# Optimization experiments

Hardware: AMD Instinct MI355X
Metric: run time of the kernel (lower is better)

## Reference

```python
import jax, jax.numpy as jnp
import numpy as np


def setup_inputs() -> dict:
    key = jax.random.key(0)
    k1, k2 = jax.random.split(key)
    x = jax.random.normal(k1, (64, 32, 32, 128), dtype=jnp.float32)
    embeddings = jax.random.normal(k2, (128, 1024), dtype=jnp.float32)  # (embedding_dim, num_embeddings)
    return {"x": x, "embeddings": embeddings}


def reference(x, embeddings):
    d = embeddings.shape[0]
    flat = x.reshape(-1, d)  # [N, d]
    # squared L2 distances: ||f||^2 + ||e||^2 - 2 f.e
    similarity = flat @ embeddings  # [N, K]
    distances = (jnp.sum(flat * flat, axis=1, keepdims=True)
                 + jnp.sum(embeddings * embeddings, axis=0)
                 - 2.0 * similarity)
    idx = jnp.argmin(distances, axis=1)  # [N]
    # gather codes (equivalent to one_hot @ embeddings^T)
    quantized = embeddings.T[idx].reshape(x.shape)
    # straight-through estimator
    quantized = x + jax.lax.stop_gradient(quantized - x)
    return quantized
```

## Files before the change

kernel.cpp:

```cpp
#include <hip/hip_runtime.h>


#define NROWS 65536
#define DDIM 128
#define KCODES 1024
#define MARGIN1 0.30f
#define MARGIN2 1e-3f

typedef __attribute__((ext_vector_type(8))) short short8;
typedef __attribute__((ext_vector_type(16))) float f32x16;

__device__ inline ushort f2bf(float f) {
    union { float f; unsigned u; } v; v.f = f;
    unsigned r = v.u + 0x7fffu + ((v.u >> 16) & 1u);
    return (ushort)(r >> 16);
}
__device__ inline float bf2f(ushort b) {
    union { unsigned u; float f; } v; v.u = ((unsigned)b) << 16;
    return v.f;
}

__device__ inline void gload_lds16(const uint4* g, uint4* lds) {
    __builtin_amdgcn_global_load_lds((const __attribute__((address_space(1))) void*)g,
                                     (__attribute__((address_space(3))) void*)lds,
                                     16, 0, 0);
}

__global__ void k_prep(const float* __restrict__ x, const float* __restrict__ e,
                       float* __restrict__ et, float* __restrict__ nrm,
                       double* __restrict__ nrm64, uint4* __restrict__ epq,
                       unsigned* __restrict__ nhl, uint4* __restrict__ xp) {
    const int gid = blockIdx.x * blockDim.x + threadIdx.x;

    {
        int lane = gid & 63, c = (gid >> 6) & 7, rt = gid >> 9;
        int row = rt * 32 + (lane & 31);
        int kbase = c * 16 + ((lane >> 5) << 3);
        const float4* xr4 = reinterpret_cast<const float4*>(x + (size_t)row * DDIM + kbase);
        float4 u = xr4[0], v = xr4[1];
        float fv[8] = {u.x, u.y, u.z, u.w, v.x, v.y, v.z, v.w};
        union { ushort s[8]; uint4 q; } pk;
        #pragma unroll
        for (int j = 0; j < 8; ++j) pk.s[j] = f2bf(fv[j]);
        xp[gid] = pk.q;
    }

    if (gid < 131072) {
        int d = gid >> 10, k = gid & 1023;
        et[k * DDIM + d] = e[gid];
    }

    if (gid < 16384) {
        int lane = gid & 63, c = (gid >> 6) & 7, nt = gid >> 9;
        int col = nt * 32 + (lane & 31);
        int kbase = c * 16 + ((lane >> 5) << 3);
        union { ushort s[8]; uint4 q; } pk;
        #pragma unroll
        for (int j = 0; j < 8; ++j)
            pk.s[j] = f2bf(e[(kbase + j) * KCODES + col]);
        epq[(size_t)nt * 512 + c * 64 + lane] = pk.q;
    }

    if (gid >= 32768 && gid < 32768 + 8192) {
        int t2 = gid - 32768;
        int k = t2 >> 3, part = t2 & 7;
        double s = 0.0;
        #pragma unroll
        for (int j = 0; j < 16; ++j) {
            double v = (double)e[(part * 16 + j) * KCODES + k];
            s = fma(v, v, s);
        }
        #pragma unroll
        for (int m = 1; m < 8; m <<= 1) s += __shfl_xor(s, m);
        if (part == 0) {
            nrm64[k] = s; nrm[k] = (float)s;
            float t0 = (float)(-0.5 * s);
            ushort hb = f2bf(t0);
            ushort lb = f2bf(t0 - bf2f(hb));
            nhl[k] = (unsigned)hb | ((unsigned)lb << 16);
        }
    }
}

__global__ __launch_bounds__(256, 3) void k_argmin32(const uint4* __restrict__ xp,
                                                     const uint4* __restrict__ epq,
                                                     const unsigned* __restrict__ nhl,
                                                     unsigned* __restrict__ pb1,
                                                     float* __restrict__ pb2) {
    __shared__ uint4 sbuf[2048];
    __shared__ unsigned snhl[128];

    const int tid = threadIdx.x;
    const int lane = tid & 63;
    const int w = tid >> 6;
    const int kq = blockIdx.x & 7;
    const int rt = (blockIdx.x >> 3) * 4 + w;
    const int lrow = lane & 31;
    const int lgrp = lane >> 5;

    #pragma unroll
    for (int i = 0; i < 8; ++i)
        gload_lds16(epq + (size_t)kq * 2048 + i * 256 + tid,
                    &sbuf[i * 256 + (w << 6)]);
    if (tid < 32)
        gload_lds16(reinterpret_cast<const uint4*>(nhl) + kq * 32 + tid,
                    reinterpret_cast<uint4*>(snhl) + tid);

    short8 ah[8];
    #pragma unroll
    for (int c = 0; c < 8; ++c) {
        union { uint4 q; short8 s; } u;
        u.q = xp[(size_t)rt * 512 + c * 64 + lane];
        ah[c] = u.s;
    }
    short8 bx = {0, 0, 0, 0, 0, 0, 0, 0};
    if (lgrp == 0) { bx[0] = (short)0x3F80; bx[1] = (short)0x3F80; }

    int cidlow[16];
    #pragma unroll
    for (int r = 0; r < 16; ++r)
        cidlow[r] = (((r & 3) + ((r >> 2) << 3)) | (lgrp << 2));

    asm volatile("s_waitcnt vmcnt(0)" ::: "memory");
    __syncthreads();

    float kb1 = -3.4e38f, kb2 = -3.4e38f;

    for (int t = 0; t < 4; ++t) {
        f32x16 acc;
        #pragma unroll
        for (int r = 0; r < 16; ++r) acc[r] = 0.f;

        #pragma unroll
        for (int c = 0; c < 8; ++c) {
            union { uint4 q; short8 s; } ef;
            ef.q = sbuf[t * 512 + c * 64 + lane];
            acc = __builtin_amdgcn_mfma_f32_32x32x16_bf16(ef.s, ah[c], acc, 0, 0, 0);
        }
        unsigned hl = snhl[t * 32 + lrow];
        short8 ax = {0, 0, 0, 0, 0, 0, 0, 0};
        if (lgrp == 0) { ax[0] = (short)(hl & 0xFFFF); ax[1] = (short)(hl >> 16); }
        acc = __builtin_amdgcn_mfma_f32_32x32x16_bf16(ax, bx, acc, 0, 0, 0);

        #pragma unroll
        for (int r = 0; r < 16; ++r) {
            unsigned cid = (unsigned)((t << 5) | cidlow[r]);
            float key = __uint_as_float((__float_as_uint(acc[r]) & 0xFFFFFF00u) | cid);
            kb2 = fmaxf(kb2, fminf(key, kb1));
            kb1 = fmaxf(kb1, key);
        }
    }

    float o1 = __shfl_xor(kb1, 32);
    float o2 = __shfl_xor(kb2, 32);
    float m1k = fmaxf(kb1, o1);
    float m2k = fmaxf(fmaxf(kb2, o2), fminf(kb1, o1));

    if (lane < 32) {
        size_t o = (size_t)kq * NROWS + rt * 32 + lrow;
        pb1[o] = __float_as_uint(m1k);
        pb2[o] = m2k;
    }
}

__global__ void k_merge(const unsigned* __restrict__ pb1, const float* __restrict__ pb2,
                        int* __restrict__ idx, int* __restrict__ wlc,
                        int* __restrict__ wl) {
    int r = blockIdx.x * blockDim.x + threadIdx.x;
    float best = -3.4e38f, sec = -3.4e38f; int bq = 0;
    #pragma unroll
    for (int q = 0; q < 8; ++q) {
        float k1 = __uint_as_float(pb1[(size_t)q * NROWS + r]);
        float k2 = pb2[(size_t)q * NROWS + r];
        bool t = k1 > best;
        sec = fmaxf(sec, fmaxf(k2, t ? best : k1));
        bq = t ? q : bq;
        best = t ? k1 : best;
    }
    unsigned ub = __float_as_uint(best);
    int code = bq * 128 + (int)(ub & 255u);
    float m1 = __uint_as_float(ub & 0xFFFFFF00u);
    float m2 = __uint_as_float(__float_as_uint(sec) & 0xFFFFFF00u);
    idx[r] = code;
    if (2.f * (m1 - m2) < MARGIN1) {
        int slot = atomicAdd(wlc, 1);
        wl[slot] = r;
    }
}

__global__ __launch_bounds__(256) void k_rescan(const float* __restrict__ x,
                                                const float* __restrict__ e,
                                                const float* __restrict__ nrm,
                                                const int* __restrict__ wlc,
                                                const int* __restrict__ wl,
                                                int* __restrict__ idx,
                                                int* __restrict__ wl2c,
                                                int* __restrict__ wl2) {
    __shared__ float xs[4][DDIM];
    __shared__ float rb1[4][256], rb2[4][256];
    __shared__ int   ri[4][256];
    const int tid = threadIdx.x, lane = tid & 63, wv = tid >> 6;
    const int n = *wlc;

    for (int i0 = blockIdx.x * 4; i0 < n; i0 += gridDim.x * 4) {
        if (tid < 128) {
            int j = tid >> 5, d4 = tid & 31;
            int ii = i0 + j;
            int row = wl[ii < n ? ii : i0];
            *reinterpret_cast<float4*>(&xs[j][d4 * 4]) =
                *reinterpret_cast<const float4*>(&x[(size_t)row * DDIM + d4 * 4]);
        }
        __syncthreads();

        float acc[4][4];
        #pragma unroll
        for (int kk = 0; kk < 4; ++kk)
            #pragma unroll
            for (int j = 0; j < 4; ++j) acc[kk][j] = 0.f;

        for (int d = 0; d < DDIM; d += 2) {
            float xv0[4], xv1[4];
            #pragma unroll
            for (int j = 0; j < 4; ++j) { xv0[j] = xs[j][d]; xv1[j] = xs[j][d + 1]; }
            #pragma unroll
            for (int kk = 0; kk < 4; ++kk) {
                float ev0 = e[d * KCODES + kk * 256 + tid];
                float ev1 = e[(d + 1) * KCODES + kk * 256 + tid];
                #pragma unroll
                for (int j = 0; j < 4; ++j) {
                    acc[kk][j] = fmaf(ev0, xv0[j], acc[kk][j]);
                    acc[kk][j] = fmaf(ev1, xv1[j], acc[kk][j]);
                }
            }
        }

        #pragma unroll
        for (int j = 0; j < 4; ++j) {
            float b1 = 3.4e38f, b2 = 3.4e38f; int bi = 0;
            #pragma unroll
            for (int kk = 0; kk < 4; ++kk) {
                int k = kk * 256 + tid;
                float s = fmaf(-2.f, acc[kk][j], nrm[k]);
                if (s < b1) { b2 = b1; b1 = s; bi = k; }
                else b2 = fminf(b2, s);
            }
            rb1[j][tid] = b1; rb2[j][tid] = b2; ri[j][tid] = bi;
        }
        __syncthreads();

        {
            float b1 = 3.4e38f, b2 = 3.4e38f; int bi = 0;
            #pragma unroll
            for (int p = 0; p < 4; ++p) {
                int t2 = lane + p * 64;
                float o1 = rb1[wv][t2], o2 = rb2[wv][t2]; int oi = ri[wv][t2];
                bool take = (o1 < b1) || (o1 == b1 && oi < bi);
                float loser = take ? b1 : o1;
                b1 = take ? o1 : b1;
                bi = take ? oi : bi;
                b2 = fminf(fminf(b2, o2), loser);
            }
            #pragma unroll
            for (int m = 1; m < 64; m <<= 1) {
                float o1 = __shfl_xor(b1, m);
                float o2 = __shfl_xor(b2, m);
                int   oi = __shfl_xor(bi, m);
                bool take = (o1 < b1) || (o1 == b1 && oi < bi);
                float loser = take ? b1 : o1;
                b1 = take ? o1 : b1;
                bi = take ? oi : bi;
                b2 = fminf(fminf(b2, o2), loser);
            }
            if (lane == 0 && i0 + wv < n) {
                int row = wl[i0 + wv];
                idx[row] = bi;
                if (b2 - b1 < MARGIN2) {
                    int slot = atomicAdd(wl2c, 1);
                    wl2[slot] = row;
                }
            }
        }
        __syncthreads();
    }
}

__global__ __launch_bounds__(256) void k_fix(const float* __restrict__ x,
                                             const float* __restrict__ e,
                                             const double* __restrict__ nrm64,
                                             const int* __restrict__ wlc,
                                             const int* __restrict__ wl,
                                             int* __restrict__ idx) {
    __shared__ float  xs[DDIM];
    __shared__ double w1[4]; __shared__ int wi[4];
    const int tid = threadIdx.x;
    const int lane = tid & 63;
    const int wv = tid >> 6;
    const int n = *wlc;

    for (int i = blockIdx.x; i < n; i += gridDim.x) {
        const int row = wl[i];
        if (tid < DDIM) xs[tid] = x[(size_t)row * DDIM + tid];
        __syncthreads();

        double dot[4] = {0.0, 0.0, 0.0, 0.0};
        for (int d0 = 0; d0 < DDIM; d0 += 8) {
            float ef[8][4];
            #pragma unroll
            for (int dd = 0; dd < 8; ++dd)
                #pragma unroll
                for (int kk = 0; kk < 4; ++kk)
                    ef[dd][kk] = e[(d0 + dd) * KCODES + tid + kk * 256];
            #pragma unroll
            for (int dd = 0; dd < 8; ++dd) {
                double xv = (double)xs[d0 + dd];
                #pragma unroll
                for (int kk = 0; kk < 4; ++kk)
                    dot[kk] = fma(xv, (double)ef[dd][kk], dot[kk]);
            }
        }

        double bb1 = 1e300; int bbi = 0;
        #pragma unroll
        for (int kk = 0; kk < 4; ++kk) {
            int k = tid + kk * 256;
            double sc = nrm64[k] - 2.0 * dot[kk];
            if (sc < bb1) { bb1 = sc; bbi = k; }
        }
        #pragma unroll
        for (int m = 1; m < 64; m <<= 1) {
            double o1 = __shfl_xor(bb1, m);
            int    oi = __shfl_xor(bbi, m);
            bool take = (o1 < bb1) || (o1 == bb1 && oi < bbi);
            bb1 = take ? o1 : bb1;
            bbi = take ? oi : bbi;
        }
        if (lane == 0) { w1[wv] = bb1; wi[wv] = bbi; }
        __syncthreads();
        if (tid == 0) {
            double f1 = w1[0]; int fi = wi[0];
            #pragma unroll
            for (int j = 1; j < 4; ++j) {
                bool take = (w1[j] < f1) || (w1[j] == f1 && wi[j] < fi);
                f1 = take ? w1[j] : f1;
                fi = take ? wi[j] : fi;
            }
            idx[row] = fi;
        }
        __syncthreads();
    }
}

__global__ void k_gather(const float* __restrict__ x, const float* __restrict__ et,
                         const int* __restrict__ idxp, float* __restrict__ out) {
    int gid = blockIdx.x * blockDim.x + threadIdx.x;
    int row = gid >> 5, d4 = gid & 31;
    float4 q = reinterpret_cast<const float4*>(et)[(size_t)idxp[row] * 32 + d4];
    float4 xv = reinterpret_cast<const float4*>(x)[gid];
    float4 o;
    o.x = xv.x + (q.x - xv.x);
    o.y = xv.y + (q.y - xv.y);
    o.z = xv.z + (q.z - xv.z);
    o.w = xv.w + (q.w - xv.w);
    reinterpret_cast<float4*>(out)[gid] = o;
}

extern "C" void kernel_launch(void* const* d_in, const int* in_sizes, int n_in,
                              void* d_out, int out_size, void* d_ws, size_t ws_size,
                              hipStream_t stream) {
    const float* x = (const float*)d_in[0];
    const float* e = (const float*)d_in[1];
    float* out = (float*)d_out;

    double*   nrm64 = (double*)d_ws;
    float*    et    = (float*)d_ws + 2048;
    float*    nrm   = et + 131072;
    int*      idx   = (int*)(nrm + 1024);
    int*      wlc   = idx + NROWS;
    int*      wl    = wlc + 4;
    int*      wl2   = wl + NROWS;
    uint4*    epq   = (uint4*)(wl2 + NROWS);
    unsigned* nhl   = (unsigned*)(epq + 16384);
    unsigned* pb1   = nhl + 1024;
    float*    pb2   = (float*)(pb1 + 8 * NROWS);
    uint4*    xp    = (uint4*)d_out;

    hipMemsetAsync(wlc, 0, 2 * sizeof(int), stream);

    k_prep<<<4096, 256, 0, stream>>>(x, e, et, nrm, nrm64, epq, nhl, xp);
    k_argmin32<<<4096, 256, 0, stream>>>(xp, epq, nhl, pb1, pb2);
    k_merge<<<NROWS / 256, 256, 0, stream>>>(pb1, pb2, idx, wlc, wl);
    k_rescan<<<768, 256, 0, stream>>>(x, e, nrm, wlc, wl, idx, wlc + 1, wl2);
    k_fix<<<64, 256, 0, stream>>>(x, e, nrm64, wlc + 1, wl2, idx);
    k_gather<<<(NROWS * 32) / 256, 256, 0, stream>>>(x, et, idx, out);
}
```

Baseline: 101.7 us.

## Process two row tiles per wave in argmin and merge rescan with fp64 fix

The MFMA argmin kernel now computes two 32-row tiles per wave. Each codebook fragment read from LDS is reused across both tiles, and the grid is halved. The single-precision rescan and the separate fp64 fix kernel are merged into one fp64 rescan, which removes a launch and the second worklist. The counter memset is folded into the prep kernel. In exchange, every rescanned row now does double-precision work, and the argmin kernel needs more registers per wave.

New measurement: 95.35 us. -6.2%, faster.

```diff
diff --git a/kernel.cpp b/kernel.cpp
--- a/kernel.cpp
+++ b/kernel.cpp
@@ -5,7 +5,6 @@
 #define DDIM 128
 #define KCODES 1024
 #define MARGIN1 0.30f
-#define MARGIN2 1e-3f
 
 typedef __attribute__((ext_vector_type(8))) short short8;
 typedef __attribute__((ext_vector_type(16))) float f32x16;
@@ -29,8 +28,11 @@
 __global__ void k_prep(const float* __restrict__ x, const float* __restrict__ e,
                        float* __restrict__ et, float* __restrict__ nrm,
                        double* __restrict__ nrm64, uint4* __restrict__ epq,
-                       unsigned* __restrict__ nhl, uint4* __restrict__ xp) {
+                       unsigned* __restrict__ nhl, uint4* __restrict__ xp,
+                       int* __restrict__ wlc) {
     const int gid = blockIdx.x * blockDim.x + threadIdx.x;
+
+    if (gid == 0) { wlc[0] = 0; wlc[1] = 0; }
 
     {
         int lane = gid & 63, c = (gid >> 6) & 7, rt = gid >> 9;
@@ -94,7 +96,9 @@
     const int lane = tid & 63;
     const int w = tid >> 6;
     const int kq = blockIdx.x & 7;
-    const int rt = (blockIdx.x >> 3) * 4 + w;
+    const int rg = blockIdx.x >> 3;
+    const int rtA = rg * 8 + w * 2;
+    const int rtB = rtA + 1;
     const int lrow = lane & 31;
     const int lgrp = lane >> 5;
 
@@ -104,14 +108,15 @@
                     &sbuf[i * 256 + (w << 6)]);
     if (tid < 32)
         gload_lds16(reinterpret_cast<const uint4*>(nhl) + kq * 32 + tid,
-                    reinterpret_cast<uint4*>(snhl) + tid);
-
-    short8 ah[8];
+                    reinterpret_cast<uint4*>(snhl));
+
+    short8 ahA[8], ahB[8];
     #pragma unroll
     for (int c = 0; c < 8; ++c) {
-        union { uint4 q; short8 s; } u;
-        u.q = xp[(size_t)rt * 512 + c * 64 + lane];
-        ah[c] = u.s;
+        union { uint4 q; short8 s; } ua, ub;
+        ua.q = xp[(size_t)rtA * 512 + c * 64 + lane];
+        ub.q = xp[(size_t)rtB * 512 + c * 64 + lane];
+        ahA[c] = ua.s; ahB[c] = ub.s;
     }
     short8 bx = {0, 0, 0, 0, 0, 0, 0, 0};
     if (lgrp == 0) { bx[0] = (short)0x3F80; bx[1] = (short)0x3F80; }
@@ -124,42 +129,60 @@
     asm volatile("s_waitcnt vmcnt(0)" ::: "memory");
     __syncthreads();
 
-    float kb1 = -3.4e38f, kb2 = -3.4e38f;
+    float kA1 = -3.4e38f, kA2 = -3.4e38f;
+    float kB1 = -3.4e38f, kB2 = -3.4e38f;
 
     for (int t = 0; t < 4; ++t) {
-        f32x16 acc;
-        #pragma unroll
-        for (int r = 0; r < 16; ++r) acc[r] = 0.f;
+        f32x16 aA, aB;
+        #pragma unroll
+        for (int r = 0; r < 16; ++r) { aA[r] = 0.f; aB[r] = 0.f; }
 
         #pragma unroll
         for (int c = 0; c < 8; ++c) {
             union { uint4 q; short8 s; } ef;
             ef.q = sbuf[t * 512 + c * 64 + lane];
-            acc = __builtin_amdgcn_mfma_f32_32x32x16_bf16(ef.s, ah[c], acc, 0, 0, 0);
+            aA = __builtin_amdgcn_mfma_f32_32x32x16_bf16(ef.s, ahA[c], aA, 0, 0, 0);
+            aB = __builtin_amdgcn_mfma_f32_32x32x16_bf16(ef.s, ahB[c], aB, 0, 0, 0);
         }
         unsigned hl = snhl[t * 32 + lrow];
         short8 ax = {0, 0, 0, 0, 0, 0, 0, 0};
         if (lgrp == 0) { ax[0] = (short)(hl & 0xFFFF); ax[1] = (short)(hl >> 16); }
-        acc = __builtin_amdgcn_mfma_f32_32x32x16_bf16(ax, bx, acc, 0, 0, 0);
+        aA = __builtin_amdgcn_mfma_f32_32x32x16_bf16(ax, bx, aA, 0, 0, 0);
+        aB = __builtin_amdgcn_mfma_f32_32x32x16_bf16(ax, bx, aB, 0, 0, 0);
 
         #pragma unroll
         for (int r = 0; r < 16; ++r) {
             unsigned cid = (unsigned)((t << 5) | cidlow[r]);
-            float key = __uint_as_float((__float_as_uint(acc[r]) & 0xFFFFFF00u) | cid);
-            kb2 = fmaxf(kb2, fminf(key, kb1));
-            kb1 = fmaxf(kb1, key);
-        }
-    }
-
-    float o1 = __shfl_xor(kb1, 32);
-    float o2 = __shfl_xor(kb2, 32);
-    float m1k = fmaxf(kb1, o1);
-    float m2k = fmaxf(fmaxf(kb2, o2), fminf(kb1, o1));
-
-    if (lane < 32) {
-        size_t o = (size_t)kq * NROWS + rt * 32 + lrow;
-        pb1[o] = __float_as_uint(m1k);
-        pb2[o] = m2k;
+            float keyA = __uint_as_float((__float_as_uint(aA[r]) & 0xFFFFFF00u) | cid);
+            float keyB = __uint_as_float((__float_as_uint(aB[r]) & 0xFFFFFF00u) | cid);
+            kA2 = fmaxf(kA2, fminf(keyA, kA1));
+            kA1 = fmaxf(kA1, keyA);
+            kB2 = fmaxf(kB2, fminf(keyB, kB1));
+            kB1 = fmaxf(kB1, keyB);
+        }
+    }
+
+    {
+        float o1 = __shfl_xor(kA1, 32);
+        float o2 = __shfl_xor(kA2, 32);
+        float m1 = fmaxf(kA1, o1);
+        float m2 = fmaxf(fmaxf(kA2, o2), fminf(kA1, o1));
+        if (lane < 32) {
+            size_t o = (size_t)kq * NROWS + rtA * 32 + lrow;
+            pb1[o] = __float_as_uint(m1);
+            pb2[o] = m2;
+        }
+    }
+    {
+        float o1 = __shfl_xor(kB1, 32);
+        float o2 = __shfl_xor(kB2, 32);
+        float m1 = fmaxf(kB1, o1);
+        float m2 = fmaxf(fmaxf(kB2, o2), fminf(kB1, o1));
+        if (lane < 32) {
+            size_t o = (size_t)kq * NROWS + rtB * 32 + lrow;
+            pb1[o] = __float_as_uint(m1);
+            pb2[o] = m2;
+        }
     }
 }
 
@@ -190,15 +213,13 @@
 
 __global__ __launch_bounds__(256) void k_rescan(const float* __restrict__ x,
                                                 const float* __restrict__ e,
-                                                const float* __restrict__ nrm,
+                                                const double* __restrict__ nrm64,
                                                 const int* __restrict__ wlc,
                                                 const int* __restrict__ wl,
-                                                int* __restrict__ idx,
-                                                int* __restrict__ wl2c,
-                                                int* __restrict__ wl2) {
-    __shared__ float xs[4][DDIM];
-    __shared__ float rb1[4][256], rb2[4][256];
-    __shared__ int   ri[4][256];
+                                                int* __restrict__ idx) {
+    __shared__ float  xs[4][DDIM];
+    __shared__ double rb1[4][256];
+    __shared__ int    ri[4][256];
     const int tid = threadIdx.x, lane = tid & 63, wv = tid >> 6;
     const int n = *wlc;
 
@@ -212,139 +233,64 @@
         }
         __syncthreads();
 
-        float acc[4][4];
+        double acc[4][4];
         #pragma unroll
         for (int kk = 0; kk < 4; ++kk)
             #pragma unroll
-            for (int j = 0; j < 4; ++j) acc[kk][j] = 0.f;
+            for (int j = 0; j < 4; ++j) acc[kk][j] = 0.0;
 
         for (int d = 0; d < DDIM; d += 2) {
-            float xv0[4], xv1[4];
-            #pragma unroll
-            for (int j = 0; j < 4; ++j) { xv0[j] = xs[j][d]; xv1[j] = xs[j][d + 1]; }
+            double xv0[4], xv1[4];
+            #pragma unroll
+            for (int j = 0; j < 4; ++j) {
+                xv0[j] = (double)xs[j][d];
+                xv1[j] = (double)xs[j][d + 1];
+            }
             #pragma unroll
             for (int kk = 0; kk < 4; ++kk) {
-                float ev0 = e[d * KCODES + kk * 256 + tid];
-                float ev1 = e[(d + 1) * KCODES + kk * 256 + tid];
+                double ev0 = (double)e[d * KCODES + kk * 256 + tid];
+                double ev1 = (double)e[(d + 1) * KCODES + kk * 256 + tid];
                 #pragma unroll
                 for (int j = 0; j < 4; ++j) {
-                    acc[kk][j] = fmaf(ev0, xv0[j], acc[kk][j]);
-                    acc[kk][j] = fmaf(ev1, xv1[j], acc[kk][j]);
+                    acc[kk][j] = fma(ev0, xv0[j], acc[kk][j]);
+                    acc[kk][j] = fma(ev1, xv1[j], acc[kk][j]);
                 }
             }
         }
 
         #pragma unroll
         for (int j = 0; j < 4; ++j) {
-            float b1 = 3.4e38f, b2 = 3.4e38f; int bi = 0;
+            double b1 = 1e300; int bi = 0;
             #pragma unroll
             for (int kk = 0; kk < 4; ++kk) {
                 int k = kk * 256 + tid;
-                float s = fmaf(-2.f, acc[kk][j], nrm[k]);
-                if (s < b1) { b2 = b1; b1 = s; bi = k; }
-                else b2 = fminf(b2, s);
-            }
-            rb1[j][tid] = b1; rb2[j][tid] = b2; ri[j][tid] = bi;
+                double s = nrm64[k] - 2.0 * acc[kk][j];
+                if (s < b1) { b1 = s; bi = k; }
+            }
+            rb1[j][tid] = b1; ri[j][tid] = bi;
         }
         __syncthreads();
 
         {
-            float b1 = 3.4e38f, b2 = 3.4e38f; int bi = 0;
+            double b1 = 1e300; int bi = 0x7FFFFFFF;
             #pragma unroll
             for (int p = 0; p < 4; ++p) {
                 int t2 = lane + p * 64;
-                float o1 = rb1[wv][t2], o2 = rb2[wv][t2]; int oi = ri[wv][t2];
+                double o1 = rb1[wv][t2]; int oi = ri[wv][t2];
                 bool take = (o1 < b1) || (o1 == b1 && oi < bi);
-                float loser = take ? b1 : o1;
                 b1 = take ? o1 : b1;
                 bi = take ? oi : bi;
-                b2 = fminf(fminf(b2, o2), loser);
             }
             #pragma unroll
             for (int m = 1; m < 64; m <<= 1) {
-                float o1 = __shfl_xor(b1, m);
-                float o2 = __shfl_xor(b2, m);
-                int   oi = __shfl_xor(bi, m);
+                double o1 = __shfl_xor(b1, m);
+                int    oi = __shfl_xor(bi, m);
                 bool take = (o1 < b1) || (o1 == b1 && oi < bi);
-                float loser = take ? b1 : o1;
                 b1 = take ? o1 : b1;
                 bi = take ? oi : bi;
-                b2 = fminf(fminf(b2, o2), loser);
-            }
-            if (lane == 0 && i0 + wv < n) {
-                int row = wl[i0 + wv];
-                idx[row] = bi;
-                if (b2 - b1 < MARGIN2) {
-                    int slot = atomicAdd(wl2c, 1);
-                    wl2[slot] = row;
-                }
-            }
-        }
-        __syncthreads();
-    }
-}
-
-__global__ __launch_bounds__(256) void k_fix(const float* __restrict__ x,
-                                             const float* __restrict__ e,
-                                             const double* __restrict__ nrm64,
-                                             const int* __restrict__ wlc,
-                                             const int* __restrict__ wl,
-                                             int* __restrict__ idx) {
-    __shared__ float  xs[DDIM];
-    __shared__ double w1[4]; __shared__ int wi[4];
-    const int tid = threadIdx.x;
-    const int lane = tid & 63;
-    const int wv = tid >> 6;
-    const int n = *wlc;
-
-    for (int i = blockIdx.x; i < n; i += gridDim.x) {
-        const int row = wl[i];
-        if (tid < DDIM) xs[tid] = x[(size_t)row * DDIM + tid];
-        __syncthreads();
-
-        double dot[4] = {0.0, 0.0, 0.0, 0.0};
-        for (int d0 = 0; d0 < DDIM; d0 += 8) {
-            float ef[8][4];
-            #pragma unroll
-            for (int dd = 0; dd < 8; ++dd)
-                #pragma unroll
-                for (int kk = 0; kk < 4; ++kk)
-                    ef[dd][kk] = e[(d0 + dd) * KCODES + tid + kk * 256];
-            #pragma unroll
-            for (int dd = 0; dd < 8; ++dd) {
-                double xv = (double)xs[d0 + dd];
-                #pragma unroll
-                for (int kk = 0; kk < 4; ++kk)
-                    dot[kk] = fma(xv, (double)ef[dd][kk], dot[kk]);
-            }
-        }
-
-        double bb1 = 1e300; int bbi = 0;
-        #pragma unroll
-        for (int kk = 0; kk < 4; ++kk) {
-            int k = tid + kk * 256;
-            double sc = nrm64[k] - 2.0 * dot[kk];
-            if (sc < bb1) { bb1 = sc; bbi = k; }
-        }
-        #pragma unroll
-        for (int m = 1; m < 64; m <<= 1) {
-            double o1 = __shfl_xor(bb1, m);
-            int    oi = __shfl_xor(bbi, m);
-            bool take = (o1 < bb1) || (o1 == bb1 && oi < bbi);
-            bb1 = take ? o1 : bb1;
-            bbi = take ? oi : bbi;
-        }
-        if (lane == 0) { w1[wv] = bb1; wi[wv] = bbi; }
-        __syncthreads();
-        if (tid == 0) {
-            double f1 = w1[0]; int fi = wi[0];
-            #pragma unroll
-            for (int j = 1; j < 4; ++j) {
-                bool take = (w1[j] < f1) || (w1[j] == f1 && wi[j] < fi);
-                f1 = take ? w1[j] : f1;
-                fi = take ? wi[j] : fi;
-            }
-            idx[row] = fi;
+            }
+            if (lane == 0 && i0 + wv < n)
+                idx[wl[i0 + wv]] = bi;
         }
         __syncthreads();
     }
@@ -377,19 +323,15 @@
     int*      idx   = (int*)(nrm + 1024);
     int*      wlc   = idx + NROWS;
     int*      wl    = wlc + 4;
-    int*      wl2   = wl + NROWS;
-    uint4*    epq   = (uint4*)(wl2 + NROWS);
+    uint4*    epq   = (uint4*)(wl + NROWS);
     unsigned* nhl   = (unsigned*)(epq + 16384);
     unsigned* pb1   = nhl + 1024;
     float*    pb2   = (float*)(pb1 + 8 * NROWS);
     uint4*    xp    = (uint4*)d_out;
 
-    hipMemsetAsync(wlc, 0, 2 * sizeof(int), stream);
-
-    k_prep<<<4096, 256, 0, stream>>>(x, e, et, nrm, nrm64, epq, nhl, xp);
-    k_argmin32<<<4096, 256, 0, stream>>>(xp, epq, nhl, pb1, pb2);
+    k_prep<<<4096, 256, 0, stream>>>(x, e, et, nrm, nrm64, epq, nhl, xp, wlc);
+    k_argmin32<<<2048, 256, 0, stream>>>(xp, epq, nhl, pb1, pb2);
     k_merge<<<NROWS / 256, 256, 0, stream>>>(pb1, pb2, idx, wlc, wl);
-    k_rescan<<<768, 256, 0, stream>>>(x, e, nrm, wlc, wl, idx, wlc + 1, wl2);
-    k_fix<<<64, 256, 0, stream>>>(x, e, nrm64, wlc + 1, wl2, idx);
+    k_rescan<<<1024, 256, 0, stream>>>(x, e, nrm64, wlc, wl, idx);
     k_gather<<<(NROWS * 32) / 256, 256, 0, stream>>>(x, et, idx, out);
 }
```
